# Kernel tuning notes

Measured on AMD Instinct MI355X. Metric: run time of the kernel, lower is better.

## Reference

```python
import jax, jax.numpy as jnp
import numpy as np

NUM_NODES = 100000
EMB_DIM = 64
OUT_C = 64
K = 3
NUM_EDGES = 1600000


def setup_inputs() -> dict:
    key = jax.random.key(0)
    k1, k2, k3, k4 = jax.random.split(key, 4)
    x_indices = jnp.arange(NUM_NODES, dtype=jnp.int64)
    ei = jax.random.randint(k1, (2, NUM_EDGES), 0, NUM_NODES, dtype=jnp.int64)
    # learned params: embedding table + final linear of SGConv
    emb_weight = jax.random.normal(k2, (NUM_NODES, EMB_DIM), dtype=jnp.float32)
    lin_w = jax.random.normal(k3, (OUT_C, EMB_DIM), dtype=jnp.float32) / np.sqrt(EMB_DIM)
    lin_b = jax.random.normal(k4, (OUT_C,), dtype=jnp.float32) * 0.01
    return {"x_indices": x_indices, "ei": ei, "emb_weight": emb_weight,
            "lin_w": lin_w, "lin_b": lin_b}


def _sgconv(x, ei, lin_w, lin_b, k_hops):
    """PyG SGConv: (D^-1/2 (A+I) D^-1/2)^K X, then Linear."""
    n = x.shape[0]
    row, col = ei[0], ei[1]
    loops = jnp.arange(n, dtype=ei.dtype)
    row = jnp.concatenate([row, loops])
    col = jnp.concatenate([col, loops])
    ones = jnp.ones(row.shape[0], dtype=x.dtype)
    deg = jax.ops.segment_sum(ones, col, num_segments=n)  # in-degree incl. self-loops
    dinv = jnp.where(deg > 0, jax.lax.rsqrt(deg), 0.0)
    norm = dinv[row] * dinv[col]  # [E+N]
    for _ in range(k_hops):
        # gather source features, scale, scatter-add to targets
        x = jax.ops.segment_sum(x[row] * norm[:, None], col, num_segments=n)
    return x @ lin_w.T + lin_b


def reference(x_indices, ei, emb_weight, lin_w, lin_b):
    x = emb_weight[x_indices]  # [N, EMB_DIM] embedding lookup
    return _sgconv(x, ei, lin_w, lin_b, K)
```

## Files before the change

### kernel.cpp

```cpp
#include <hip/hip_runtime.h>
#include <hip/hip_bf16.h>
#include <math.h>


#define FLAG_MX 0
#define FLAG_ME 1
#define SH 9
#define WC 512
#define CH 4096
#define RMASK 0x7FFFFFu

using short8 = __attribute__((ext_vector_type(8))) short;
using f32x4 = __attribute__((ext_vector_type(4))) float;

__device__ inline int idx_at(const void* p, long long i, int mode) {
    switch (mode) {
        case 1: return (int)((const long long*)p)[i];
        case 2: return (int)((const float*)p)[i];
        case 3: return (int)((const double*)p)[i];
        default: return ((const int*)p)[i];
    }
}

__device__ inline unsigned short f2bf(float f) {
    union { float f; unsigned u; } v; v.f = f;
    unsigned r = v.u + 0x7FFFu + ((v.u >> 16) & 1u);
    return (unsigned short)(r >> 16);
}
__device__ inline float bflo(unsigned d) { union { unsigned u; float f; } v; v.u = d << 16; return v.f; }
__device__ inline float bfhi(unsigned d) { union { unsigned u; float f; } v; v.u = d & 0xFFFF0000u; return v.f; }
__device__ inline unsigned pk(float a, float b) {
    return (unsigned)f2bf(a) | ((unsigned)f2bf(b) << 16);
}

__device__ int detect_me_block(const void* ei, int n, int* sbuf) {
    int t = threadIdx.x;
    int oke = 15;
    const int* w = (const int*)ei;
    const long long* L = (const long long*)ei;
    const float* f = (const float*)ei;
    const double* d = (const double*)ei;
    for (int k = t; k < 2048; k += 256) {
        if (!((unsigned)w[k] < (unsigned)n)) oke &= ~1;
        long long lv = L[k];
        if (!(lv >= 0 && lv < (long long)n)) oke &= ~2;
        float fv = f[k];
        if (!(fv >= 0.f && fv < (float)n && fv == truncf(fv))) oke &= ~4;
        double dv = d[k];
        if (!(dv >= 0.0 && dv < (double)n && dv == trunc(dv))) oke &= ~8;
    }
    sbuf[t] = oke;
    __syncthreads();
    for (int st = 128; st; st >>= 1) {
        if (t < st) sbuf[t] &= sbuf[t + st];
        __syncthreads();
    }
    int r = sbuf[0];
    __syncthreads();
    return (r & 2) ? 1 : (r & 8) ? 3 : (r & 4) ? 2 : 0;
}

__device__ int detect_mx_block(const void* xidx, int* sbuf) {
    int t = threadIdx.x;
    int okx = 15;
    const int* w = (const int*)xidx;
    const long long* L = (const long long*)xidx;
    const float* f = (const float*)xidx;
    const double* d = (const double*)xidx;
    for (int k = t; k < 2048; k += 256) {
        if (w[k] != k) okx &= ~1;
        if (L[k] != (long long)k) okx &= ~2;
        if (!(f[k] == (float)k)) okx &= ~4;
        if (!(d[k] == (double)k)) okx &= ~8;
    }
    sbuf[t] = okx;
    __syncthreads();
    for (int st = 128; st; st >>= 1) {
        if (t < st) sbuf[t] &= sbuf[t + st];
        __syncthreads();
    }
    int r = sbuf[0];
    __syncthreads();
    return (r & 2) ? 1 : (r & 8) ? 3 : (r & 4) ? 2 : 0;
}

__global__ void __launch_bounds__(256) k_p1(
        const void* __restrict__ ei, const void* __restrict__ xidx,
        long long E, int n, int NBUK, int NBLK,
        int* __restrict__ bhist, int* __restrict__ flags) {
    __shared__ int hist[256];
    __shared__ int sbuf[256];
    int t = threadIdx.x;
    int blk = blockIdx.x;
    int me = detect_me_block(ei, n, sbuf);
    if (blk == 0) {
        int mx = detect_mx_block(xidx, sbuf);
        if (t == 0) { flags[FLAG_ME] = me; flags[FLAG_MX] = mx; }
    }
    long long base = (long long)blk * CH;
    int cnt = (int)min((long long)CH, E - base);
    hist[t] = 0;
    __syncthreads();
    for (int i = t; i < cnt; i += 256) {
        int c = idx_at(ei, E + base + i, me);
        int b = min(c >> SH, NBUK - 1);
        atomicAdd(&hist[b], 1);
    }
    __syncthreads();
    if (t < NBUK) bhist[(size_t)t * NBLK + blk] = hist[t];
}

__global__ void __launch_bounds__(256) k_p2a(
        int* __restrict__ bhist, int* __restrict__ gcount, int NBLK, int NBUK,
        const float* __restrict__ w, unsigned short* __restrict__ w8) {
    __shared__ int s[256];
    int b = blockIdx.x;
    int t = threadIdx.x;
    if (b >= NBUK) {
        for (int i = t; i < 4096; i += 256) w8[i] = f2bf(w[i]);
        return;
    }
    int* row = bhist + (size_t)b * NBLK;
    int carry = 0;
    for (int base = 0; base < NBLK; base += 256) {
        int i = base + t;
        int v = (i < NBLK) ? row[i] : 0;
        s[t] = v;
        __syncthreads();
        for (int st = 1; st < 256; st <<= 1) {
            int add = (t >= st) ? s[t - st] : 0;
            __syncthreads();
            s[t] += add;
            __syncthreads();
        }
        if (i < NBLK) row[i] = carry + s[t] - v;
        int total = s[255];
        __syncthreads();
        carry += total;
    }
    if (t == 0) gcount[b] = carry;
}

__device__ void scan_gcount(const int* gcount, int NBUK, int* p, int* gb_ex) {
    int t = threadIdx.x;
    int v = (t < NBUK) ? gcount[t] : 0;
    p[t] = v;
    __syncthreads();
    for (int st = 1; st < 256; st <<= 1) {
        int add = (t >= st) ? p[t - st] : 0;
        __syncthreads();
        p[t] += add;
        __syncthreads();
    }
    gb_ex[t] = p[t] - v;
    __syncthreads();
}

__device__ void scan_gcount_512(const int* gcount, int NBUK, int* p, int* gb_ex) {
    int t = threadIdx.x;
    int v = (t < 256) ? ((t < NBUK) ? gcount[t] : 0) : 0;
    if (t < 256) p[t] = v;
    __syncthreads();
    for (int st = 1; st < 256; st <<= 1) {
        int add = (t >= st && t < 256) ? p[t - st] : 0;
        __syncthreads();
        if (t < 256) p[t] += add;
        __syncthreads();
    }
    if (t < 256) gb_ex[t] = p[t] - v;
    __syncthreads();
}

__global__ void __launch_bounds__(256) k_p3(
        const void* __restrict__ ei, long long E, int n, int NBUK, int NBLK,
        const int* __restrict__ bhist, const int* __restrict__ gcount,
        unsigned* __restrict__ gstag, const int* __restrict__ flags) {
    __shared__ int hist[256], lbase[256], rsv[256], lcur[256], s[256], gb[256];
    __shared__ unsigned stage[CH];
    int t = threadIdx.x;
    int blk = blockIdx.x;
    scan_gcount(gcount, NBUK, s, gb);
    long long base = (long long)blk * CH;
    int cnt = (int)min((long long)CH, E - base);
    int me = flags[FLAG_ME];
    hist[t] = 0;
    __syncthreads();
    for (int i = t; i < cnt; i += 256) {
        int c = idx_at(ei, E + base + i, me);
        atomicAdd(&hist[min(c >> SH, NBUK - 1)], 1);
    }
    __syncthreads();
    int v = hist[t];
    s[t] = v;
    __syncthreads();
    for (int st = 1; st < 256; st <<= 1) {
        int add = (t >= st) ? s[t - st] : 0;
        __syncthreads();
        s[t] += add;
        __syncthreads();
    }
    lbase[t] = s[t] - v;
    lcur[t] = s[t] - v;
    if (t < NBUK) rsv[t] = gb[t] + bhist[(size_t)t * NBLK + blk];
    __syncthreads();
    for (int i = t; i < cnt; i += 256) {
        long long e = base + i;
        int r = idx_at(ei, e, me);
        int c = idx_at(ei, E + e, me);
        int b = min(c >> SH, NBUK - 1);
        unsigned pkv = ((unsigned)r & RMASK) |
                       (((unsigned)(c - (b << SH)) & (WC - 1)) << 23);
        int slot = atomicAdd(&lcur[b], 1);
        stage[slot] = pkv;
    }
    __syncthreads();
    for (int i = t; i < cnt; i += 256) {
        unsigned pkv = stage[i];
        int lo = 0, hi = NBUK - 1;
        while (lo < hi) {
            int mid = (lo + hi + 1) >> 1;
            if (lbase[mid] <= i) lo = mid; else hi = mid - 1;
        }
        gstag[rsv[lo] + (i - lbase[lo])] = pkv;
    }
}

__global__ void __launch_bounds__(512) k_p4(
        const unsigned* __restrict__ gstag, const int* __restrict__ gcount,
        int* __restrict__ off, float* __restrict__ dinv,
        int* __restrict__ rowidx, int n, int NBUK) {
    __shared__ int hist[WC], lofs[WC], cur[WC], p[512], gb[256];
    int t = threadIdx.x;
    int b = blockIdx.x;
    int cbase = b << SH;
    scan_gcount_512(gcount, NBUK, p, gb);
    int e0 = gb[b];
    int e1 = e0 + gcount[b];
    int cnt = e1 - e0;
    if (b == NBUK - 1 && t == 0) off[n] = e1;
    hist[t] = 0;
    __syncthreads();
    for (int i = t; i < cnt; i += 512) {
        atomicAdd(&hist[gstag[e0 + i] >> 23], 1);
    }
    __syncthreads();
    int v = hist[t];
    p[t] = v;
    __syncthreads();
    for (int st = 1; st < 512; st <<= 1) {
        int add = (t >= st) ? p[t - st] : 0;
        __syncthreads();
        p[t] += add;
        __syncthreads();
    }
    int excl = p[t] - v;
    lofs[t] = excl;
    cur[t] = excl;
    __syncthreads();
    int ncols = n - cbase;
    if (ncols < 0) ncols = 0;
    if (ncols > WC) ncols = WC;
    if (t < ncols) {
        off[cbase + t] = e0 + lofs[t];
        dinv[cbase + t] = rsqrtf((float)(hist[t] + 1));
    }
    for (int i = t; i < cnt; i += 512) {
        unsigned pkv = gstag[e0 + i];
        int cl = (int)(pkv >> 23);
        int slot = atomicAdd(&cur[cl], 1);
        rowidx[e0 + slot] = (int)(pkv & RMASK);
    }
}

__global__ void __launch_bounds__(256) k_z0(
        const void* __restrict__ xidx, const float4* __restrict__ emb4,
        const float* __restrict__ dinv, uint4* __restrict__ z, int n,
        const int* __restrict__ flags) {
    int i = blockIdx.x * 256 + threadIdx.x;
    if (i >= n * 8) return;
    int node = i >> 3, q = i & 7;
    int xi = idx_at(xidx, node, flags[FLAG_MX]);
    if ((unsigned)xi >= (unsigned)n) xi = 0;
    float d = dinv[node];
    float4 a = emb4[(long long)xi * 16 + q * 2];
    float4 b = emb4[(long long)xi * 16 + q * 2 + 1];
    uint4 o;
    o.x = pk(a.x * d, a.y * d);
    o.y = pk(a.z * d, a.w * d);
    o.z = pk(b.x * d, b.y * d);
    o.w = pk(b.z * d, b.w * d);
    z[(long long)node * 8 + q] = o;
}

__device__ inline void acc8(float* acc, uint4 s) {
    acc[0] += bflo(s.x); acc[1] += bfhi(s.x);
    acc[2] += bflo(s.y); acc[3] += bfhi(s.y);
    acc[4] += bflo(s.z); acc[5] += bfhi(s.z);
    acc[6] += bflo(s.w); acc[7] += bfhi(s.w);
}

__global__ void __launch_bounds__(256) k_hop(
        const uint4* __restrict__ zin, uint4* __restrict__ zout,
        const float* __restrict__ dinv, const int* __restrict__ off,
        const int* __restrict__ rowidx, int n) {
    int tid = blockIdx.x * 256 + threadIdx.x;
    int node = tid >> 3;
    int q = tid & 7;
    if (node >= n) return;
    float acc[8];
    {
        uint4 s = zin[(long long)node * 8 + q];
        acc[0] = bflo(s.x); acc[1] = bfhi(s.x);
        acc[2] = bflo(s.y); acc[3] = bfhi(s.y);
        acc[4] = bflo(s.z); acc[5] = bfhi(s.z);
        acc[6] = bflo(s.w); acc[7] = bfhi(s.w);
    }
    int e0 = off[node], e1 = off[node + 1];
    int e = e0;
    for (; e + 4 <= e1; e += 4) {
        int r0 = rowidx[e + 0];
        int r1 = rowidx[e + 1];
        int r2 = rowidx[e + 2];
        int r3 = rowidx[e + 3];
        uint4 s0 = zin[(long long)r0 * 8 + q];
        uint4 s1 = zin[(long long)r1 * 8 + q];
        uint4 s2 = zin[(long long)r2 * 8 + q];
        uint4 s3 = zin[(long long)r3 * 8 + q];
        acc8(acc, s0);
        acc8(acc, s1);
        acc8(acc, s2);
        acc8(acc, s3);
    }
    for (; e < e1; e++) {
        int r = rowidx[e];
        acc8(acc, zin[(long long)r * 8 + q]);
    }
    float d = dinv[node];
    float sc = d * d;
    uint4 o;
    o.x = pk(acc[0] * sc, acc[1] * sc);
    o.y = pk(acc[2] * sc, acc[3] * sc);
    o.z = pk(acc[4] * sc, acc[5] * sc);
    o.w = pk(acc[6] * sc, acc[7] * sc);
    zout[(long long)node * 8 + q] = o;
}

__global__ void __launch_bounds__(256) k_hop3_lin(
        const uint4* __restrict__ zin, const float* __restrict__ dinv,
        const int* __restrict__ off, const int* __restrict__ rowidx,
        const unsigned short* __restrict__ w8, const float* __restrict__ bias,
        float* __restrict__ out, int n) {
    __shared__ uint4 z3[32][8];
    int t = threadIdx.x;
    int l = t >> 3;
    int q = t & 7;
    int node = blockIdx.x * 32 + l;
    uint4 o = {0u, 0u, 0u, 0u};
    if (node < n) {
        float acc[8];
        {
            uint4 s = zin[(long long)node * 8 + q];
            acc[0] = bflo(s.x); acc[1] = bfhi(s.x);
            acc[2] = bflo(s.y); acc[3] = bfhi(s.y);
            acc[4] = bflo(s.z); acc[5] = bfhi(s.z);
            acc[6] = bflo(s.w); acc[7] = bfhi(s.w);
        }
        int e0 = off[node], e1 = off[node + 1];
        int e = e0;
        for (; e + 4 <= e1; e += 4) {
            int r0 = rowidx[e + 0];
            int r1 = rowidx[e + 1];
            int r2 = rowidx[e + 2];
            int r3 = rowidx[e + 3];
            uint4 s0 = zin[(long long)r0 * 8 + q];
            uint4 s1 = zin[(long long)r1 * 8 + q];
            uint4 s2 = zin[(long long)r2 * 8 + q];
            uint4 s3 = zin[(long long)r3 * 8 + q];
            acc8(acc, s0);
            acc8(acc, s1);
            acc8(acc, s2);
            acc8(acc, s3);
        }
        for (; e < e1; e++) {
            int r = rowidx[e];
            acc8(acc, zin[(long long)r * 8 + q]);
        }
        float d = dinv[node];
        o.x = pk(acc[0] * d, acc[1] * d);
        o.y = pk(acc[2] * d, acc[3] * d);
        o.z = pk(acc[4] * d, acc[5] * d);
        o.w = pk(acc[6] * d, acc[7] * d);
    }
    z3[l][q ^ (l & 7)] = o;
    __syncthreads();

    int lane = t & 63, wv = t >> 6;
    int tile = wv >> 1;
    int nh = wv & 1;
    int col = lane & 15, quad = lane >> 4;
    int node0 = blockIdx.x * 32 + tile * 16;
    int ln = tile * 16 + col;
    short8 a[2];
#pragma unroll
    for (int s = 0; s < 2; s++) {
        int c = s * 4 + quad;
        a[s] = *(const short8*)&z3[ln][c ^ (ln & 7)];
    }
    const short8* wp = (const short8*)w8;
#pragma unroll
    for (int j = 0; j < 2; j++) {
        int tN = nh * 2 + j;
        float bv = bias[tN * 16 + col];
        f32x4 acc4 = {bv, bv, bv, bv};
        acc4 = __builtin_amdgcn_mfma_f32_16x16x32_bf16(
            a[0], wp[(tN * 16 + col) * 8 + 0 * 4 + quad], acc4, 0, 0, 0);
        acc4 = __builtin_amdgcn_mfma_f32_16x16x32_bf16(
            a[1], wp[(tN * 16 + col) * 8 + 1 * 4 + quad], acc4, 0, 0, 0);
#pragma unroll
        for (int r = 0; r < 4; r++) {
            int nd = node0 + quad * 4 + r;
            if (nd < n) out[(size_t)nd * 64 + tN * 16 + col] = acc4[r];
        }
    }
}

extern "C" void kernel_launch(void* const* d_in, const int* in_sizes, int n_in,
                              void* d_out, int out_size, void* d_ws, size_t ws_size,
                              hipStream_t stream) {
    const void* xidx = d_in[0];
    const void* ei = d_in[1];
    const float* emb = (const float*)d_in[2];
    const float* w = (const float*)d_in[3];
    const float* b = (const float*)d_in[4];

    const int n = in_sizes[0];
    const long long E = in_sizes[1] / 2;
    int NBUK = (int)((n + WC - 1) >> SH);
    if (NBUK > 256) NBUK = 256;
    const int NBLK = (int)((E + CH - 1) / CH);

    char* p = (char*)d_ws;
    auto alloc = [&](size_t bytes) -> void* {
        void* r = (void*)p;
        p += (bytes + 255) & ~(size_t)255;
        return r;
    };
    int* flags = (int*)alloc(256);
    float* dinv = (float*)alloc((size_t)n * 4);
    int* off = (int*)alloc((size_t)(n + 1) * 4);
    int* gcount = (int*)alloc(257 * 4);
    int* bhist = (int*)alloc((size_t)NBLK * NBUK * 4);
    int* rowidx = (int*)alloc((size_t)E * 4);
    uint4* zA = (uint4*)alloc((size_t)n * 64 * 2);
    unsigned short* w8 = (unsigned short*)alloc(4096 * 2);
    uint4* zS = (uint4*)d_out;

    unsigned* gstag;
    if ((size_t)E * 4 <= (size_t)n * 64 * 2)
        gstag = (unsigned*)((char*)d_out + (size_t)n * 64 * 2);
    else
        gstag = (unsigned*)alloc((size_t)E * 4);

    k_p1<<<NBLK, 256, 0, stream>>>(ei, xidx, E, n, NBUK, NBLK, bhist, flags);
    k_p2a<<<NBUK + 1, 256, 0, stream>>>(bhist, gcount, NBLK, NBUK, w, w8);
    k_p3<<<NBLK, 256, 0, stream>>>(ei, E, n, NBUK, NBLK, bhist, gcount, gstag, flags);
    k_p4<<<NBUK, 512, 0, stream>>>(gstag, gcount, off, dinv, rowidx, n, NBUK);

    const int gF = (n * 8 + 255) / 256;
    const int gL = (n + 31) / 32;

    k_z0<<<gF, 256, 0, stream>>>(xidx, (const float4*)emb, dinv, zA, n, flags);
    k_hop<<<gF, 256, 0, stream>>>(zA, zS, dinv, off, rowidx, n);
    k_hop<<<gF, 256, 0, stream>>>(zS, zA, dinv, off, rowidx, n);
    k_hop3_lin<<<gL, 256, 0, stream>>>(zA, dinv, off, rowidx, w8, b,
                                       (float*)d_out, n);
}
```

Baseline: 250.5 us.

## Sort CSR neighbor lists and gather in source-range passes for cache locality

Sorts each node's neighbor list in the CSR build with a per-column insertion sort. The hop kernels then walk sources in several ascending range passes (about 25.6K nodes each), so concurrent threads gather from the same slice of the feature table, which is meant to improve L2/MALL hit rates. Index loads and output stores become nontemporal. The cost is a serial insertion sort per column in the build kernel, plus extra branching and pass loops in the gather, which may cause divergence.

```diff
diff --git a/kernel.cpp b/kernel.cpp
--- a/kernel.cpp
+++ b/kernel.cpp
@@ -12,6 +12,7 @@
 
 using short8 = __attribute__((ext_vector_type(8))) short;
 using f32x4 = __attribute__((ext_vector_type(4))) float;
+using uint32x4 = __attribute__((ext_vector_type(4))) unsigned;
 
 __device__ inline int idx_at(const void* p, long long i, int mode) {
     switch (mode) {
@@ -269,6 +270,20 @@
         int cl = (int)(pkv >> 23);
         int slot = atomicAdd(&cur[cl], 1);
         rowidx[e0 + slot] = (int)(pkv & RMASK);
+    }
+    __syncthreads();
+    if (t < ncols) {
+        int s0 = e0 + lofs[t];
+        int s1 = s0 + hist[t];
+        for (int i = s0 + 1; i < s1; i++) {
+            int key = rowidx[i];
+            int j = i - 1;
+            while (j >= s0 && rowidx[j] > key) {
+                rowidx[j + 1] = rowidx[j];
+                j--;
+            }
+            rowidx[j + 1] = key;
+        }
     }
 }
 
@@ -299,57 +314,76 @@
     acc[6] += bflo(s.w); acc[7] += bfhi(s.w);
 }
 
+__device__ inline void hop_body(
+        float* acc, const uint4* __restrict__ zin,
+        const int* __restrict__ rowidx, int e, int e1,
+        int node, int q, int n, int npass) {
+#pragma unroll 8
+    for (int i = 0; i < 8; i++) acc[i] = 0.f;
+    int prev = 0;
+    for (int pass = 0; pass < npass; pass++) {
+        int bound = (pass == npass - 1)
+                        ? n
+                        : (int)(((long long)(pass + 1) * n) / npass);
+        if (node >= prev && node < bound) {
+            uint4 s = zin[(long long)node * 8 + q];
+            acc8(acc, s);
+        }
+        while (e < e1) {
+            if (e + 4 <= e1) {
+                int r3 = __builtin_nontemporal_load(rowidx + e + 3);
+                if (r3 < bound) {
+                    int r0 = __builtin_nontemporal_load(rowidx + e + 0);
+                    int r1 = __builtin_nontemporal_load(rowidx + e + 1);
+                    int r2 = __builtin_nontemporal_load(rowidx + e + 2);
+                    uint4 s0 = zin[(long long)r0 * 8 + q];
+                    uint4 s1 = zin[(long long)r1 * 8 + q];
+                    uint4 s2 = zin[(long long)r2 * 8 + q];
+                    uint4 s3 = zin[(long long)r3 * 8 + q];
+                    acc8(acc, s0);
+                    acc8(acc, s1);
+                    acc8(acc, s2);
+                    acc8(acc, s3);
+                    e += 4;
+                    continue;
+                }
+            }
+            int r = __builtin_nontemporal_load(rowidx + e);
+            if (r >= bound) break;
+            acc8(acc, zin[(long long)r * 8 + q]);
+            e++;
+        }
+        prev = bound;
+    }
+}
+
 __global__ void __launch_bounds__(256) k_hop(
         const uint4* __restrict__ zin, uint4* __restrict__ zout,
         const float* __restrict__ dinv, const int* __restrict__ off,
-        const int* __restrict__ rowidx, int n) {
+        const int* __restrict__ rowidx, int n, int npass) {
     int tid = blockIdx.x * 256 + threadIdx.x;
     int node = tid >> 3;
     int q = tid & 7;
     if (node >= n) return;
+    int e0 = off[node], e1 = off[node + 1];
     float acc[8];
-    {
-        uint4 s = zin[(long long)node * 8 + q];
-        acc[0] = bflo(s.x); acc[1] = bfhi(s.x);
-        acc[2] = bflo(s.y); acc[3] = bfhi(s.y);
-        acc[4] = bflo(s.z); acc[5] = bfhi(s.z);
-        acc[6] = bflo(s.w); acc[7] = bfhi(s.w);
-    }
-    int e0 = off[node], e1 = off[node + 1];
-    int e = e0;
-    for (; e + 4 <= e1; e += 4) {
-        int r0 = rowidx[e + 0];
-        int r1 = rowidx[e + 1];
-        int r2 = rowidx[e + 2];
-        int r3 = rowidx[e + 3];
-        uint4 s0 = zin[(long long)r0 * 8 + q];
-        uint4 s1 = zin[(long long)r1 * 8 + q];
-        uint4 s2 = zin[(long long)r2 * 8 + q];
-        uint4 s3 = zin[(long long)r3 * 8 + q];
-        acc8(acc, s0);
-        acc8(acc, s1);
-        acc8(acc, s2);
-        acc8(acc, s3);
-    }
-    for (; e < e1; e++) {
-        int r = rowidx[e];
-        acc8(acc, zin[(long long)r * 8 + q]);
-    }
+    hop_body(acc, zin, rowidx, e0, e1, node, q, n, npass);
     float d = dinv[node];
     float sc = d * d;
-    uint4 o;
-    o.x = pk(acc[0] * sc, acc[1] * sc);
-    o.y = pk(acc[2] * sc, acc[3] * sc);
-    o.z = pk(acc[4] * sc, acc[5] * sc);
-    o.w = pk(acc[6] * sc, acc[7] * sc);
-    zout[(long long)node * 8 + q] = o;
+    uint32x4 o;
+    o[0] = pk(acc[0] * sc, acc[1] * sc);
+    o[1] = pk(acc[2] * sc, acc[3] * sc);
+    o[2] = pk(acc[4] * sc, acc[5] * sc);
+    o[3] = pk(acc[6] * sc, acc[7] * sc);
+    __builtin_nontemporal_store(
+        o, (uint32x4*)&zout[(long long)node * 8 + q]);
 }
 
 __global__ void __launch_bounds__(256) k_hop3_lin(
         const uint4* __restrict__ zin, const float* __restrict__ dinv,
         const int* __restrict__ off, const int* __restrict__ rowidx,
         const unsigned short* __restrict__ w8, const float* __restrict__ bias,
-        float* __restrict__ out, int n) {
+        float* __restrict__ out, int n, int npass) {
     __shared__ uint4 z3[32][8];
     int t = threadIdx.x;
     int l = t >> 3;
@@ -357,34 +391,9 @@
     int node = blockIdx.x * 32 + l;
     uint4 o = {0u, 0u, 0u, 0u};
     if (node < n) {
+        int e0 = off[node], e1 = off[node + 1];
         float acc[8];
-        {
-            uint4 s = zin[(long long)node * 8 + q];
-            acc[0] = bflo(s.x); acc[1] = bfhi(s.x);
-            acc[2] = bflo(s.y); acc[3] = bfhi(s.y);
-            acc[4] = bflo(s.z); acc[5] = bfhi(s.z);
-            acc[6] = bflo(s.w); acc[7] = bfhi(s.w);
-        }
-        int e0 = off[node], e1 = off[node + 1];
-        int e = e0;
-        for (; e + 4 <= e1; e += 4) {
-            int r0 = rowidx[e + 0];
-            int r1 = rowidx[e + 1];
-            int r2 = rowidx[e + 2];
-            int r3 = rowidx[e + 3];
-            uint4 s0 = zin[(long long)r0 * 8 + q];
-            uint4 s1 = zin[(long long)r1 * 8 + q];
-            uint4 s2 = zin[(long long)r2 * 8 + q];
-            uint4 s3 = zin[(long long)r3 * 8 + q];
-            acc8(acc, s0);
-            acc8(acc, s1);
-            acc8(acc, s2);
-            acc8(acc, s3);
-        }
-        for (; e < e1; e++) {
-            int r = rowidx[e];
-            acc8(acc, zin[(long long)r * 8 + q]);
-        }
+        hop_body(acc, zin, rowidx, e0, e1, node, q, n, npass);
         float d = dinv[node];
         o.x = pk(acc[0] * d, acc[1] * d);
         o.y = pk(acc[2] * d, acc[3] * d);
@@ -438,6 +447,9 @@
     int NBUK = (int)((n + WC - 1) >> SH);
     if (NBUK > 256) NBUK = 256;
     const int NBLK = (int)((E + CH - 1) / CH);
+
+    int npass = (n + 25599) / 25600;
+    if (npass < 1) npass = 1;
 
     char* p = (char*)d_ws;
     auto alloc = [&](size_t bytes) -> void* {
@@ -470,8 +482,8 @@
     const int gL = (n + 31) / 32;
 
     k_z0<<<gF, 256, 0, stream>>>(xidx, (const float4*)emb, dinv, zA, n, flags);
-    k_hop<<<gF, 256, 0, stream>>>(zA, zS, dinv, off, rowidx, n);
-    k_hop<<<gF, 256, 0, stream>>>(zS, zA, dinv, off, rowidx, n);
+    k_hop<<<gF, 256, 0, stream>>>(zA, zS, dinv, off, rowidx, n, npass);
+    k_hop<<<gF, 256, 0, stream>>>(zS, zA, dinv, off, rowidx, n, npass);
     k_hop3_lin<<<gL, 256, 0, stream>>>(zA, dinv, off, rowidx, w8, b,
-                                       (float*)d_out, n);
-}
+                                       (float*)d_out, n, npass);
+}
```

Result: slower. 463.1 us (+84.9%).

## Split each node's edge list across two 8-lane groups with shuffle reduction

Applied to the files above, without the earlier changes.

Each hop kernel now assigns 16 threads per node instead of 8. The edge range is split into two halves, each half is accumulated by its own group of 8 lanes, and the partial sums are combined with a cross-lane xor-shuffle. This doubles the thread count and memory-level parallelism for the irregular gathers, at the cost of more threads, the shuffles, and idle lanes during the write. The final hop+linear kernel now handles 16 nodes per block, so each wave computes one 16-column output tile.

```diff
diff --git a/kernel.cpp b/kernel.cpp
--- a/kernel.cpp
+++ b/kernel.cpp
@@ -299,25 +299,26 @@
     acc[6] += bflo(s.w); acc[7] += bfhi(s.w);
 }
 
-__global__ void __launch_bounds__(256) k_hop(
-        const uint4* __restrict__ zin, uint4* __restrict__ zout,
-        const float* __restrict__ dinv, const int* __restrict__ off,
-        const int* __restrict__ rowidx, int n) {
-    int tid = blockIdx.x * 256 + threadIdx.x;
-    int node = tid >> 3;
-    int q = tid & 7;
-    if (node >= n) return;
-    float acc[8];
-    {
+__device__ inline void hop_half(
+        float* acc, const uint4* __restrict__ zin,
+        const int* __restrict__ rowidx, int node, int h, int q,
+        const int* __restrict__ off) {
+    if (h == 0) {
         uint4 s = zin[(long long)node * 8 + q];
         acc[0] = bflo(s.x); acc[1] = bfhi(s.x);
         acc[2] = bflo(s.y); acc[3] = bfhi(s.y);
         acc[4] = bflo(s.z); acc[5] = bfhi(s.z);
         acc[6] = bflo(s.w); acc[7] = bfhi(s.w);
+    } else {
+#pragma unroll 8
+        for (int i = 0; i < 8; i++) acc[i] = 0.f;
     }
     int e0 = off[node], e1 = off[node + 1];
-    int e = e0;
-    for (; e + 4 <= e1; e += 4) {
+    int half = (e1 - e0 + 1) >> 1;
+    int lo = e0 + h * half;
+    int hi = h ? e1 : (e0 + half);
+    int e = lo;
+    for (; e + 4 <= hi; e += 4) {
         int r0 = rowidx[e + 0];
         int r1 = rowidx[e + 1];
         int r2 = rowidx[e + 2];
@@ -331,18 +332,35 @@
         acc8(acc, s2);
         acc8(acc, s3);
     }
-    for (; e < e1; e++) {
+    for (; e < hi; e++) {
         int r = rowidx[e];
         acc8(acc, zin[(long long)r * 8 + q]);
     }
-    float d = dinv[node];
-    float sc = d * d;
-    uint4 o;
-    o.x = pk(acc[0] * sc, acc[1] * sc);
-    o.y = pk(acc[2] * sc, acc[3] * sc);
-    o.z = pk(acc[4] * sc, acc[5] * sc);
-    o.w = pk(acc[6] * sc, acc[7] * sc);
-    zout[(long long)node * 8 + q] = o;
+}
+
+__global__ void __launch_bounds__(256) k_hop(
+        const uint4* __restrict__ zin, uint4* __restrict__ zout,
+        const float* __restrict__ dinv, const int* __restrict__ off,
+        const int* __restrict__ rowidx, int n) {
+    int tid = blockIdx.x * 256 + threadIdx.x;
+    int node = tid >> 4;
+    if (node >= n) return;
+    int h = (tid >> 3) & 1;
+    int q = tid & 7;
+    float acc[8];
+    hop_half(acc, zin, rowidx, node, h, q, off);
+#pragma unroll 8
+    for (int i = 0; i < 8; i++) acc[i] += __shfl_xor(acc[i], 8);
+    if (h == 0) {
+        float d = dinv[node];
+        float sc = d * d;
+        uint4 o;
+        o.x = pk(acc[0] * sc, acc[1] * sc);
+        o.y = pk(acc[2] * sc, acc[3] * sc);
+        o.z = pk(acc[4] * sc, acc[5] * sc);
+        o.w = pk(acc[6] * sc, acc[7] * sc);
+        zout[(long long)node * 8 + q] = o;
+    }
 }
 
 __global__ void __launch_bounds__(256) k_hop3_lin(
@@ -350,56 +368,38 @@
         const int* __restrict__ off, const int* __restrict__ rowidx,
         const unsigned short* __restrict__ w8, const float* __restrict__ bias,
         float* __restrict__ out, int n) {
-    __shared__ uint4 z3[32][8];
-    int t = threadIdx.x;
-    int l = t >> 3;
+    __shared__ uint4 z3[16][8];
+    int t = threadIdx.x;
+    int l = t >> 4;
+    int h = (t >> 3) & 1;
     int q = t & 7;
-    int node = blockIdx.x * 32 + l;
-    uint4 o = {0u, 0u, 0u, 0u};
+    int node = blockIdx.x * 16 + l;
+    float acc[8];
     if (node < n) {
-        float acc[8];
-        {
-            uint4 s = zin[(long long)node * 8 + q];
-            acc[0] = bflo(s.x); acc[1] = bfhi(s.x);
-            acc[2] = bflo(s.y); acc[3] = bfhi(s.y);
-            acc[4] = bflo(s.z); acc[5] = bfhi(s.z);
-            acc[6] = bflo(s.w); acc[7] = bfhi(s.w);
+        hop_half(acc, zin, rowidx, node, h, q, off);
+    } else {
+#pragma unroll 8
+        for (int i = 0; i < 8; i++) acc[i] = 0.f;
+    }
+#pragma unroll 8
+    for (int i = 0; i < 8; i++) acc[i] += __shfl_xor(acc[i], 8);
+    if (h == 0) {
+        uint4 o = {0u, 0u, 0u, 0u};
+        if (node < n) {
+            float d = dinv[node];
+            o.x = pk(acc[0] * d, acc[1] * d);
+            o.y = pk(acc[2] * d, acc[3] * d);
+            o.z = pk(acc[4] * d, acc[5] * d);
+            o.w = pk(acc[6] * d, acc[7] * d);
         }
-        int e0 = off[node], e1 = off[node + 1];
-        int e = e0;
-        for (; e + 4 <= e1; e += 4) {
-            int r0 = rowidx[e + 0];
-            int r1 = rowidx[e + 1];
-            int r2 = rowidx[e + 2];
-            int r3 = rowidx[e + 3];
-            uint4 s0 = zin[(long long)r0 * 8 + q];
-            uint4 s1 = zin[(long long)r1 * 8 + q];
-            uint4 s2 = zin[(long long)r2 * 8 + q];
-            uint4 s3 = zin[(long long)r3 * 8 + q];
-            acc8(acc, s0);
-            acc8(acc, s1);
-            acc8(acc, s2);
-            acc8(acc, s3);
-        }
-        for (; e < e1; e++) {
-            int r = rowidx[e];
-            acc8(acc, zin[(long long)r * 8 + q]);
-        }
-        float d = dinv[node];
-        o.x = pk(acc[0] * d, acc[1] * d);
-        o.y = pk(acc[2] * d, acc[3] * d);
-        o.z = pk(acc[4] * d, acc[5] * d);
-        o.w = pk(acc[6] * d, acc[7] * d);
-    }
-    z3[l][q ^ (l & 7)] = o;
+        z3[l][q ^ (l & 7)] = o;
+    }
     __syncthreads();
 
     int lane = t & 63, wv = t >> 6;
-    int tile = wv >> 1;
-    int nh = wv & 1;
     int col = lane & 15, quad = lane >> 4;
-    int node0 = blockIdx.x * 32 + tile * 16;
-    int ln = tile * 16 + col;
+    int node0 = blockIdx.x * 16;
+    int ln = col;
     short8 a[2];
 #pragma unroll
     for (int s = 0; s < 2; s++) {
@@ -407,20 +407,16 @@
         a[s] = *(const short8*)&z3[ln][c ^ (ln & 7)];
     }
     const short8* wp = (const short8*)w8;
+    float bv = bias[wv * 16 + col];
+    f32x4 acc4 = {bv, bv, bv, bv};
+    acc4 = __builtin_amdgcn_mfma_f32_16x16x32_bf16(
+        a[0], wp[(wv * 16 + col) * 8 + 0 * 4 + quad], acc4, 0, 0, 0);
+    acc4 = __builtin_amdgcn_mfma_f32_16x16x32_bf16(
+        a[1], wp[(wv * 16 + col) * 8 + 1 * 4 + quad], acc4, 0, 0, 0);
 #pragma unroll
-    for (int j = 0; j < 2; j++) {
-        int tN = nh * 2 + j;
-        float bv = bias[tN * 16 + col];
-        f32x4 acc4 = {bv, bv, bv, bv};
-        acc4 = __builtin_amdgcn_mfma_f32_16x16x32_bf16(
-            a[0], wp[(tN * 16 + col) * 8 + 0 * 4 + quad], acc4, 0, 0, 0);
-        acc4 = __builtin_amdgcn_mfma_f32_16x16x32_bf16(
-            a[1], wp[(tN * 16 + col) * 8 + 1 * 4 + quad], acc4, 0, 0, 0);
-#pragma unroll
-        for (int r = 0; r < 4; r++) {
-            int nd = node0 + quad * 4 + r;
-            if (nd < n) out[(size_t)nd * 64 + tN * 16 + col] = acc4[r];
-        }
+    for (int r = 0; r < 4; r++) {
+        int nd = node0 + quad * 4 + r;
+        if (nd < n) out[(size_t)nd * 64 + wv * 16 + col] = acc4[r];
     }
 }
 
@@ -467,11 +463,12 @@
     k_p4<<<NBUK, 512, 0, stream>>>(gstag, gcount, off, dinv, rowidx, n, NBUK);
 
     const int gF = (n * 8 + 255) / 256;
-    const int gL = (n + 31) / 32;
+    const int gH = (n * 16 + 255) / 256;
+    const int gL = (n + 15) / 16;
 
     k_z0<<<gF, 256, 0, stream>>>(xidx, (const float4*)emb, dinv, zA, n, flags);
-    k_hop<<<gF, 256, 0, stream>>>(zA, zS, dinv, off, rowidx, n);
-    k_hop<<<gF, 256, 0, stream>>>(zS, zA, dinv, off, rowidx, n);
+    k_hop<<<gH, 256, 0, stream>>>(zA, zS, dinv, off, rowidx, n);
+    k_hop<<<gH, 256, 0, stream>>>(zS, zA, dinv, off, rowidx, n);
     k_hop3_lin<<<gL, 256, 0, stream>>>(zA, dinv, off, rowidx, w8, b,
                                        (float*)d_out, n);
 }
```

After: 254.6 us. Within noise of the previous version (+1.6%).
